# Kernel tuning notes

Measured on AMD Instinct MI355X. Metric: run time of the kernel, lower is better.

The kernel has to match this reference:

```python
import jax, jax.numpy as jnp
import numpy as np

IN_FEATURES = 4096
OUT_FEATURES = 4096
N_TOKENS = 8192  # flattened batch*seq


def setup_inputs() -> dict:
    key = jax.random.key(0)
    kx, kw = jax.random.split(key)
    x = jax.random.normal(kx, (N_TOKENS, IN_FEATURES), dtype=jnp.float16)
    # Full weight [out, in], split into a 2:4 structured part and the complement
    # (mirrors prune_2_to_4's [0,0,1,1] pattern along the in dim).
    W = jax.random.normal(kw, (OUT_FEATURES, IN_FEATURES), dtype=jnp.float16)
    pattern = jnp.asarray([0, 0, 1, 1], dtype=jnp.float16)
    mask = jnp.tile(pattern, IN_FEATURES // 4)  # [in]
    W_dense = W * mask          # 2:4 semi-structured component
    W_sparse = W * (1 - mask)   # unstructured CSR component (complement)
    return {"x": x, "W_dense": W_dense, "W_sparse": W_sparse}


def reference(x, W_dense, W_sparse):
    # Original: out_dense = W_semi @ x^T ; out_sparse = spmm(W_csr, x^T)
    #           out = out_sparse^T + out_dense^T
    # Equivalent: x @ W_dense^T + x @ W_sparse^T, two separate GEMMs summed.
    out_dense = jnp.einsum('ni,oi->no', x, W_dense)
    out_sparse = jnp.einsum('ni,oi->no', x, W_sparse)
    return out_dense + out_sparse
```

## Files before the change

### kernel.cpp

```cpp
#include <hip/hip_runtime.h>
#include <stdint.h>


#define NT 8192
#define NO 4096
#define NK 4096

typedef float f32x4 __attribute__((ext_vector_type(4)));
typedef _Float16 f16x8 __attribute__((ext_vector_type(8)));

__device__ __forceinline__ void gload_lds16(const void* g, void* l) {
  __builtin_amdgcn_global_load_lds(
      (const __attribute__((address_space(1))) void*)g,
      (__attribute__((address_space(3))) void*)l, 16, 0, 0);
}

#define BAR() __builtin_amdgcn_s_barrier()
#define WV6() asm volatile("s_waitcnt vmcnt(6)" ::: "memory")
#define PRIO1() __builtin_amdgcn_s_setprio(1)
#define PRIO0() __builtin_amdgcn_s_setprio(0)

__global__ __launch_bounds__(256) void cvt_all(
    const float* __restrict__ x, const float* __restrict__ wd,
    const float* __restrict__ ws, _Float16* __restrict__ xh,
    _Float16* __restrict__ wh, int nx8, int nw8) {
  int i = blockIdx.x * 256 + threadIdx.x;
  if (i < nx8) {
    const f32x4* p = (const f32x4*)x + 2 * (size_t)i;
    f32x4 lo = p[0], hi = p[1];
    f16x8 r;
#pragma unroll
    for (int j = 0; j < 4; ++j) { r[j] = (_Float16)lo[j]; r[j + 4] = (_Float16)hi[j]; }
    *((f16x8*)xh + i) = r;
  } else {
    int j8 = i - nx8;
    if (j8 < nw8) {
      const f32x4* pd = (const f32x4*)wd + 2 * (size_t)j8;
      const f32x4* ps = (const f32x4*)ws + 2 * (size_t)j8;
      f32x4 dl = pd[0], dh = pd[1], sl = ps[0], sh = ps[1];
      f16x8 r;
#pragma unroll
      for (int j = 0; j < 4; ++j) {
        r[j] = (_Float16)(dl[j] + sl[j]);
        r[j + 4] = (_Float16)(dh[j] + sh[j]);
      }
      *((f16x8*)wh + j8) = r;
    }
  }
}


#define RDA(B_, MG) do { _Pragma("unroll") \
  for (int mm = 0; mm < 4; ++mm) { \
    ar[0][mm] = *(const f16x8*)(Ab[B_] + ((MG)*8 + mm*2 + 0) * 1024 + finner); \
    ar[1][mm] = *(const f16x8*)(Ab[B_] + ((MG)*8 + mm*2 + 1) * 1024 + finner); \
  } } while (0)

#define RDB(B_, NG) do { _Pragma("unroll") \
  for (int nn = 0; nn < 2; ++nn) { \
    br[0][(NG)*2+nn] = *(const f16x8*)(Bb[B_] + ((bsub + (NG)*2 + nn)*2 + 0) * 1024 + finner); \
    br[1][(NG)*2+nn] = *(const f16x8*)(Bb[B_] + ((bsub + (NG)*2 + nn)*2 + 1) * 1024 + finner); \
  } } while (0)

#define MM(MG, NG) do { _Pragma("unroll") \
  for (int ks = 0; ks < 2; ++ks) \
    _Pragma("unroll") for (int mm = 0; mm < 4; ++mm) \
      _Pragma("unroll") for (int nn = 0; nn < 2; ++nn) \
        acc[(MG)*4+mm][(NG)*2+nn] = __builtin_amdgcn_mfma_f32_16x16x32_f16( \
            br[ks][(NG)*2+nn], ar[ks][mm], acc[(MG)*4+mm][(NG)*2+nn], 0, 0, 0); \
  } while (0)

#define STG(BUF_, OP_, H_, S_, KCOL) \
  gload_lds16(((OP_) ? Wrow : Xrow) + ((H_)*128 + (S_)*64) * NK + (KCOL), \
              ldsc + (BUF_)*65536 + (OP_)*32768 + (H_)*16384 + (S_)*8192 + t16)

__global__ __launch_bounds__(512, 2) void gemm8p(
    const _Float16* __restrict__ Xg, const _Float16* __restrict__ Wg,
    float* __restrict__ C) {
  __shared__ _Float16 lds[2][2][2][8192];
  char* ldsc = (char*)&lds[0][0][0][0];

  const int t = threadIdx.x;
  const int lane = t & 63;
  const int wv = t >> 6;
  const int wr = wv >> 2;
  const int wc = wv & 3;
  const int fr = lane & 15;
  const int kq = lane >> 4;
  const int t16 = t * 16;

  const int swz = (blockIdx.x & 7) * 64 + (blockIdx.x >> 3);
  const int bm = swz >> 4, bn = swz & 15;
  const int brow = bm * 256, bcol = bn * 256;

  const int o = t16;
  const int sub = o >> 10;
  const int inner = o & 1023;
  const int innsw = inner ^ (((inner >> 9) & 1) << 5);
  const int rloc = ((sub >> 1) << 4) | ((innsw >> 6) & 15);
  const int kloc = ((sub & 1) << 5) | ((innsw >> 1) & 31);

  const _Float16* Xrow = Xg + (brow + rloc) * NK + kloc;
  const _Float16* Wrow = Wg + (bcol + rloc) * NK + kloc;

  const int finner = ((fr << 6) | (kq << 4)) ^ ((fr & 8) << 2);
  const char* Ab[2] = { ldsc + wr * 16384, ldsc + 65536 + wr * 16384 };
  const char* Bb[2] = { ldsc + 32768 + (wc >> 1) * 16384,
                        ldsc + 65536 + 32768 + (wc >> 1) * 16384 };
  const int bsub = (wc & 1) * 4;

  f16x8 ar[2][4], br[2][4];
  f32x4 acc[8][4] = {};

  STG(0, 0, 0, 0, 0); STG(0, 0, 0, 1, 0); STG(0, 0, 1, 0, 0); STG(0, 0, 1, 1, 0);
  STG(0, 1, 0, 0, 0); STG(0, 1, 0, 1, 0); STG(0, 1, 1, 0, 0); STG(0, 1, 1, 1, 0);
  STG(1, 0, 0, 0, 64); STG(1, 0, 1, 0, 64);
  STG(1, 1, 0, 0, 64); STG(1, 1, 0, 1, 64); STG(1, 1, 1, 0, 64); STG(1, 1, 1, 1, 64);
  WV6(); BAR();

#pragma unroll 1
  for (int i = 0; i < NK / 128; ++i) {
    const int k1 = i * 128 + 64;
    const int kt2 = (i * 128 + 128) & (NK - 1);
    const int kt3 = (i * 128 + 192) & (NK - 1);

    RDA(0, 0); RDB(0, 0); RDB(0, 1);
    STG(1, 0, 0, 1, k1); STG(1, 0, 1, 1, k1);
    PRIO1(); MM(0, 0); PRIO0(); BAR();
    STG(0, 0, 0, 0, kt2); STG(0, 0, 1, 0, kt2);
    PRIO1(); MM(0, 1); PRIO0();
    RDA(0, 1);
    BAR();
    STG(0, 1, 0, 0, kt2); STG(0, 1, 0, 1, kt2);
    PRIO1(); MM(1, 0); PRIO0(); BAR();
    STG(0, 1, 1, 0, kt2); STG(0, 1, 1, 1, kt2);
    PRIO1(); MM(1, 1); PRIO0();
    WV6(); BAR();
    RDA(1, 0); RDB(1, 0); RDB(1, 1);
    STG(0, 0, 0, 1, kt2); STG(0, 0, 1, 1, kt2);
    PRIO1(); MM(0, 0); PRIO0(); BAR();

    STG(1, 0, 0, 0, kt3); STG(1, 0, 1, 0, kt3);
    PRIO1(); MM(0, 1); PRIO0();
    RDA(1, 1);
    BAR();

    STG(1, 1, 0, 0, kt3); STG(1, 1, 0, 1, kt3);
    PRIO1(); MM(1, 0); PRIO0(); BAR();

    STG(1, 1, 1, 0, kt3); STG(1, 1, 1, 1, kt3);
    PRIO1(); MM(1, 1); PRIO0();
    WV6(); BAR();
  }

  const long r0 = brow + wr * 128 + fr;
  const int c0 = bcol + wc * 64 + kq * 4;
#pragma unroll
  for (int m = 0; m < 8; ++m)
#pragma unroll
    for (int n = 0; n < 4; ++n)
      *(f32x4*)(C + (r0 + m * 16) * NO + c0 + n * 16) = acc[m][n];
}

__global__ __launch_bounds__(256) void gemm_fb(
    const float* __restrict__ Xf, const float* __restrict__ Wdf,
    const float* __restrict__ Wsf, float* __restrict__ C) {
  __shared__ _Float16 lsA[128 * 32];
  __shared__ _Float16 lsB[128 * 32];

  const int t = threadIdx.x;
  const int lane = t & 63;
  const int wid = t >> 6;
  const int wr = wid >> 1, wc = wid & 1;

  const int nwg = (NT / 128) * (NO / 128);
  const int swz = (blockIdx.x & 7) * (nwg >> 3) + (blockIdx.x >> 3);
  const int nbn = NO / 128;
  const int bm = swz / nbn, bn = swz % nbn;
  const long brow = (long)bm * 128, bcol = (long)bn * 128;

  const int srow = t >> 2;
  const int scol = (t & 3) * 8;
  const float* X  = Xf + (brow + srow) * (long)NK + scol;
  const float* Wd = Wdf + (bcol + srow) * (long)NK + scol;
  const float* Ws = Wsf + (bcol + srow) * (long)NK + scol;
  _Float16* lA = lsA + t * 8;
  _Float16* lB = lsB + t * 8;

  const int fr = lane & 15;
  const int kg = (lane >> 4) * 8;
  const _Float16* pA = lsA + (wr * 64 + fr) * 32 + kg;
  const _Float16* pB = lsB + (wc * 64 + fr) * 32 + kg;

  f32x4 acc[4][4] = {};

  for (int k0 = 0; k0 < NK; k0 += 32) {
    f32x4 aL0 = *(const f32x4*)(X + k0),  aH0 = *(const f32x4*)(X + k0 + 4);
    f32x4 aL1 = *(const f32x4*)(X + k0 + 64 * NK), aH1 = *(const f32x4*)(X + k0 + 64 * NK + 4);
    f32x4 dL0 = *(const f32x4*)(Wd + k0), dH0 = *(const f32x4*)(Wd + k0 + 4);
    f32x4 sL0 = *(const f32x4*)(Ws + k0), sH0 = *(const f32x4*)(Ws + k0 + 4);
    f32x4 dL1 = *(const f32x4*)(Wd + k0 + 64 * NK), dH1 = *(const f32x4*)(Wd + k0 + 64 * NK + 4);
    f32x4 sL1 = *(const f32x4*)(Ws + k0 + 64 * NK), sH1 = *(const f32x4*)(Ws + k0 + 64 * NK + 4);
    __syncthreads();
    f16x8 va0, va1, vb0, vb1;
#pragma unroll
    for (int j = 0; j < 4; ++j) {
      va0[j] = (_Float16)aL0[j];            va0[j + 4] = (_Float16)aH0[j];
      va1[j] = (_Float16)aL1[j];            va1[j + 4] = (_Float16)aH1[j];
      vb0[j] = (_Float16)(dL0[j] + sL0[j]); vb0[j + 4] = (_Float16)(dH0[j] + sH0[j]);
      vb1[j] = (_Float16)(dL1[j] + sL1[j]); vb1[j + 4] = (_Float16)(dH1[j] + sH1[j]);
    }
    *(f16x8*)lA = va0;
    *(f16x8*)(lA + 64 * 32) = va1;
    *(f16x8*)lB = vb0;
    *(f16x8*)(lB + 64 * 32) = vb1;
    __syncthreads();
    f16x8 af[4], bf[4];
#pragma unroll
    for (int i2 = 0; i2 < 4; ++i2) af[i2] = *(const f16x8*)(pA + i2 * 16 * 32);
#pragma unroll
    for (int i2 = 0; i2 < 4; ++i2) bf[i2] = *(const f16x8*)(pB + i2 * 16 * 32);
#pragma unroll
    for (int i2 = 0; i2 < 4; ++i2)
#pragma unroll
      for (int j2 = 0; j2 < 4; ++j2)
        acc[i2][j2] = __builtin_amdgcn_mfma_f32_16x16x32_f16(af[i2], bf[j2], acc[i2][j2], 0, 0, 0);
  }

  const int fq = lane >> 4;
#pragma unroll
  for (int i2 = 0; i2 < 4; ++i2)
#pragma unroll
    for (int j2 = 0; j2 < 4; ++j2)
#pragma unroll
      for (int r = 0; r < 4; ++r) {
        long row = brow + wr * 64 + i2 * 16 + fq * 4 + r;
        long col = bcol + wc * 64 + j2 * 16 + fr;
        C[row * NO + col] = acc[i2][j2][r];
      }
}

extern "C" void kernel_launch(void* const* d_in, const int* in_sizes, int n_in,
                              void* d_out, int out_size, void* d_ws, size_t ws_size,
                              hipStream_t stream) {
  const float* x   = (const float*)d_in[0];
  const float* wd  = (const float*)d_in[1];
  const float* wsp = (const float*)d_in[2];
  float* out = (float*)d_out;

  const size_t xh_bytes = (size_t)NT * NK * 2;
  const size_t wh_bytes = (size_t)NO * NK * 2;

  if (d_ws != nullptr && ws_size >= xh_bytes + wh_bytes) {
    _Float16* xh = (_Float16*)d_ws;
    _Float16* wh = (_Float16*)((char*)d_ws + xh_bytes);
    const int nx8 = NT * NK / 8;
    const int nw8 = NO * NK / 8;
    cvt_all<<<(nx8 + nw8) / 256, 256, 0, stream>>>(x, wd, wsp, xh, wh, nx8, nw8);
    gemm8p<<<(NT / 256) * (NO / 256), 512, 0, stream>>>(xh, wh, out);
  } else {
    gemm_fb<<<(NT / 128) * (NO / 128), 256, 0, stream>>>(x, wd, wsp, out);
  }
}
```

Measured before the change: 296.3 us.

## Switch main GEMM from 16x16x32 to 32x32x16 MFMA tiles

```diff
diff --git a/kernel.cpp b/kernel.cpp
--- a/kernel.cpp
+++ b/kernel.cpp
@@ -7,6 +7,7 @@
 #define NK 4096
 
 typedef float f32x4 __attribute__((ext_vector_type(4)));
+typedef float f32x16 __attribute__((ext_vector_type(16)));
 typedef _Float16 f16x8 __attribute__((ext_vector_type(8)));
 
 __device__ __forceinline__ void gload_lds16(const void* g, void* l) {
@@ -50,24 +51,26 @@
 }
 
 
-#define RDA(B_, MG) do { _Pragma("unroll") \
-  for (int mm = 0; mm < 4; ++mm) { \
-    ar[0][mm] = *(const f16x8*)(Ab[B_] + ((MG)*8 + mm*2 + 0) * 1024 + finner); \
-    ar[1][mm] = *(const f16x8*)(Ab[B_] + ((MG)*8 + mm*2 + 1) * 1024 + finner); \
+#define RDA32(B_, MG) do { _Pragma("unroll") \
+  for (int mtl = 0; mtl < 2; ++mtl) { \
+    const int mt = (MG) * 2 + mtl; \
+    const char* ab = Ab[B_] + (mt >> 1) * 8192; \
+    _Pragma("unroll") for (int ks = 0; ks < 4; ++ks) \
+      ar[mtl][ks] = *(const f16x8*)(ab + ((mt * 2 + lh) & 3) * 2048 + \
+          (ks >> 1) * 1024 + lbase + (lswz ^ ((ks & 1) << 5))); \
   } } while (0)
 
-#define RDB(B_, NG) do { _Pragma("unroll") \
-  for (int nn = 0; nn < 2; ++nn) { \
-    br[0][(NG)*2+nn] = *(const f16x8*)(Bb[B_] + ((bsub + (NG)*2 + nn)*2 + 0) * 1024 + finner); \
-    br[1][(NG)*2+nn] = *(const f16x8*)(Bb[B_] + ((bsub + (NG)*2 + nn)*2 + 1) * 1024 + finner); \
-  } } while (0)
-
-#define MM(MG, NG) do { _Pragma("unroll") \
-  for (int ks = 0; ks < 2; ++ks) \
-    _Pragma("unroll") for (int mm = 0; mm < 4; ++mm) \
-      _Pragma("unroll") for (int nn = 0; nn < 2; ++nn) \
-        acc[(MG)*4+mm][(NG)*2+nn] = __builtin_amdgcn_mfma_f32_16x16x32_f16( \
-            br[ks][(NG)*2+nn], ar[ks][mm], acc[(MG)*4+mm][(NG)*2+nn], 0, 0, 0); \
+#define RDB32(B_, NG) do { _Pragma("unroll") \
+  for (int ks = 0; ks < 4; ++ks) \
+    br[NG][ks] = *(const f16x8*)(Bb[B_] + ((NG) * 2 + lh) * 2048 + \
+        (ks >> 1) * 1024 + lbase + (lswz ^ ((ks & 1) << 5))); \
+  } while (0)
+
+#define MM32(MG, NG) do { _Pragma("unroll") \
+  for (int mtl = 0; mtl < 2; ++mtl) \
+    _Pragma("unroll") for (int ks = 0; ks < 4; ++ks) \
+      acc[(MG) * 2 + mtl][NG] = __builtin_amdgcn_mfma_f32_32x32x16_f16( \
+          br[NG][ks], ar[mtl][ks], acc[(MG) * 2 + mtl][NG], 0, 0, 0); \
   } while (0)
 
 #define STG(BUF_, OP_, H_, S_, KCOL) \
@@ -85,8 +88,6 @@
   const int wv = t >> 6;
   const int wr = wv >> 2;
   const int wc = wv & 3;
-  const int fr = lane & 15;
-  const int kq = lane >> 4;
   const int t16 = t * 16;
 
   const int swz = (blockIdx.x & 7) * 64 + (blockIdx.x >> 3);
@@ -103,14 +104,15 @@
   const _Float16* Xrow = Xg + (brow + rloc) * NK + kloc;
   const _Float16* Wrow = Wg + (bcol + rloc) * NK + kloc;
 
-  const int finner = ((fr << 6) | (kq << 4)) ^ ((fr & 8) << 2);
+  const int lh = (lane >> 4) & 1;
+  const int lbase = ((lane & 15) << 6) + ((lane >> 5) << 4);
+  const int lswz = (lane & 8) << 2;
   const char* Ab[2] = { ldsc + wr * 16384, ldsc + 65536 + wr * 16384 };
-  const char* Bb[2] = { ldsc + 32768 + (wc >> 1) * 16384,
-                        ldsc + 65536 + 32768 + (wc >> 1) * 16384 };
-  const int bsub = (wc & 1) * 4;
+  const char* Bb[2] = { ldsc + 32768 + (wc >> 1) * 16384 + (wc & 1) * 8192,
+                        ldsc + 65536 + 32768 + (wc >> 1) * 16384 + (wc & 1) * 8192 };
 
   f16x8 ar[2][4], br[2][4];
-  f32x4 acc[8][4] = {};
+  f32x16 acc[4][2] = {};
 
   STG(0, 0, 0, 0, 0); STG(0, 0, 0, 1, 0); STG(0, 0, 1, 0, 0); STG(0, 0, 1, 1, 0);
   STG(0, 1, 0, 0, 0); STG(0, 1, 0, 1, 0); STG(0, 1, 1, 0, 0); STG(0, 1, 1, 1, 0);
@@ -124,42 +126,47 @@
     const int kt2 = (i * 128 + 128) & (NK - 1);
     const int kt3 = (i * 128 + 192) & (NK - 1);
 
-    RDA(0, 0); RDB(0, 0); RDB(0, 1);
+    RDA32(0, 0); RDB32(0, 0);
     STG(1, 0, 0, 1, k1); STG(1, 0, 1, 1, k1);
-    PRIO1(); MM(0, 0); PRIO0(); BAR();
+    PRIO1(); MM32(0, 0); PRIO0(); BAR();
+    RDB32(0, 1);
     STG(0, 0, 0, 0, kt2); STG(0, 0, 1, 0, kt2);
-    PRIO1(); MM(0, 1); PRIO0();
-    RDA(0, 1);
-    BAR();
+    PRIO1(); MM32(0, 1); PRIO0(); BAR();
+    RDA32(0, 1);
     STG(0, 1, 0, 0, kt2); STG(0, 1, 0, 1, kt2);
-    PRIO1(); MM(1, 0); PRIO0(); BAR();
+    PRIO1(); MM32(1, 0); PRIO0(); BAR();
     STG(0, 1, 1, 0, kt2); STG(0, 1, 1, 1, kt2);
-    PRIO1(); MM(1, 1); PRIO0();
+    PRIO1(); MM32(1, 1); PRIO0();
     WV6(); BAR();
-    RDA(1, 0); RDB(1, 0); RDB(1, 1);
+    RDA32(1, 0); RDB32(1, 0);
     STG(0, 0, 0, 1, kt2); STG(0, 0, 1, 1, kt2);
-    PRIO1(); MM(0, 0); PRIO0(); BAR();
-
+    PRIO1(); MM32(0, 0); PRIO0(); BAR();
+
+    RDB32(1, 1);
     STG(1, 0, 0, 0, kt3); STG(1, 0, 1, 0, kt3);
-    PRIO1(); MM(0, 1); PRIO0();
-    RDA(1, 1);
-    BAR();
-
+    PRIO1(); MM32(0, 1); PRIO0(); BAR();
+
+    RDA32(1, 1);
     STG(1, 1, 0, 0, kt3); STG(1, 1, 0, 1, kt3);
-    PRIO1(); MM(1, 0); PRIO0(); BAR();
+    PRIO1(); MM32(1, 0); PRIO0(); BAR();
 
     STG(1, 1, 1, 0, kt3); STG(1, 1, 1, 1, kt3);
-    PRIO1(); MM(1, 1); PRIO0();
+    PRIO1(); MM32(1, 1); PRIO0();
     WV6(); BAR();
   }
 
-  const long r0 = brow + wr * 128 + fr;
-  const int c0 = bcol + wc * 64 + kq * 4;
-#pragma unroll
-  for (int m = 0; m < 8; ++m)
-#pragma unroll
-    for (int n = 0; n < 4; ++n)
-      *(f32x4*)(C + (r0 + m * 16) * NO + c0 + n * 16) = acc[m][n];
+  const long r0 = brow + wr * 128 + (lane & 31);
+  const int c0 = bcol + wc * 64 + ((lane >> 5) << 2);
+#pragma unroll
+  for (int mt = 0; mt < 4; ++mt)
+#pragma unroll
+    for (int nt = 0; nt < 2; ++nt)
+#pragma unroll
+      for (int g = 0; g < 4; ++g) {
+        f32x4 v = { acc[mt][nt][g * 4 + 0], acc[mt][nt][g * 4 + 1],
+                    acc[mt][nt][g * 4 + 2], acc[mt][nt][g * 4 + 3] };
+        *(f32x4*)(C + (r0 + mt * 32) * NO + c0 + nt * 32 + g * 8) = v;
+      }
 }
 
 __global__ __launch_bounds__(256) void gemm_fb(
```

Measured after the change: 333.8 us. +12.7%, slower.
